# Kernel optimization log

Measured on AMD Instinct MI355X. Metric: run time of the kernel, lower is better.

Reference implementation:

```python
import jax, jax.numpy as jnp
import numpy as np

B, T, C, H = 4, 4096, 1024, 64  # batch, seq_len, n_embd, head_size


def setup_inputs() -> dict:
    key = jax.random.key(0)
    kx, kk, kq, kv = jax.random.split(key, 4)
    x = jax.random.normal(kx, (B, T, C), dtype=jnp.float32)
    Wk = jax.random.normal(kk, (C, H), dtype=jnp.float32) * (C ** -0.5)
    Wq = jax.random.normal(kq, (C, H), dtype=jnp.float32) * (C ** -0.5)
    Wv = jax.random.normal(kv, (C, H), dtype=jnp.float32) * (C ** -0.5)
    return {"x": x, "Wk": Wk, "Wq": Wq, "Wv": Wv}


def reference(x, Wk, Wq, Wv):
    # q,k,v: (B,T,H)
    k = jnp.einsum('btc,ch->bth', x, Wk)
    q = jnp.einsum('btc,ch->bth', x, Wq)
    v = jnp.einsum('btc,ch->bth', x, Wv)
    # NOTE: source scales by C**-0.5 (embedding dim), not head_size**-0.5
    scale = jnp.asarray(C, x.dtype) ** -0.5
    scores = jnp.einsum('bqh,bkh->bqk', q, k) * scale  # (B,T,T)
    causal = jnp.tril(jnp.ones((T, T), dtype=bool))
    scores = jnp.where(causal, scores, jnp.asarray(-jnp.inf, scores.dtype))
    weight = jax.nn.softmax(scores, axis=-1)
    out = jnp.einsum('bqk,bkh->bqh', weight, v)  # (B,T,H)
    return out
```

## Files before the change

### kernel.cpp

```cpp
#include <hip/hip_runtime.h>

typedef unsigned short u16;
typedef unsigned int u32;
typedef float v4f __attribute__((ext_vector_type(4)));
typedef __bf16 v8bf __attribute__((ext_vector_type(8)));

__device__ __forceinline__ u16 f2bf(float f) {
    union { float f; u32 u; } v; v.f = f;
    u32 r = v.u + 0x7fffu + ((v.u >> 16) & 1u);
    return (u16)(r >> 16);
}
__device__ __forceinline__ u32 pk2(float lo, float hi) {
    return ((u32)f2bf(hi) << 16) | (u32)f2bf(lo);
}
__device__ __forceinline__ u32 pk2t(float lo, float hi) {
    union { float f; u32 u; } a, b; a.f = hi; b.f = lo;
    return __builtin_amdgcn_perm(a.u, b.u, 0x07060302u);
}
__device__ __forceinline__ float bfLo(u32 p) {
    union { u32 u; float f; } v; v.u = p << 16; return v.f;
}
__device__ __forceinline__ float bfHi(u32 p) {
    union { u32 u; float f; } v; v.u = p & 0xffff0000u; return v.f;
}
__device__ __forceinline__ v4f zero4() { v4f z = {0.f, 0.f, 0.f, 0.f}; return z; }

__global__ __launch_bounds__(64) void prep_w(const float* __restrict__ Wk,
                                             const float* __restrict__ Wq,
                                             const float* __restrict__ Wv,
                                             u16* __restrict__ WtF) {
    const int f = blockIdx.x >> 5;
    const int ks = blockIdx.x & 31;
    const int lane = threadIdx.x;
    const int w = f >> 2;
    const float* W = (w == 0) ? Wk : ((w == 1) ? Wq : Wv);
    const int h = (f & 3) * 16 + (lane & 15);
    const int k0 = ks * 32 + (lane >> 4) * 8;
    u16 tmp[8];
#pragma unroll
    for (int j = 0; j < 8; ++j) tmp[j] = f2bf(W[(size_t)(k0 + j) * 64 + h]);
    *(uint4*)&WtF[((size_t)blockIdx.x * 64 + lane) * 8] = *(const uint4*)tmp;
}

__global__ __launch_bounds__(256, 2) void qkv_proj(const float* __restrict__ x,
                                                   const u16* __restrict__ WtF,
                                                   u16* __restrict__ qgf,
                                                   u16* __restrict__ Kf,
                                                   u16* __restrict__ Vf) {
    __shared__ v4f red[3][24][64];
    u16* Tk = (u16*)&red[0][0][0];
    u16* Tq = Tk + 32 * 72;
    u16* Tv = Tq + 32 * 72;

    const int tid = threadIdx.x;
    const int lane = tid & 63;
    const int wv = tid >> 6;
    const int l15 = lane & 15, quad = lane >> 4;
    const int row0 = blockIdx.x * 32;

    v4f acc[2][12];
#pragma unroll
    for (int rh = 0; rh < 2; ++rh)
#pragma unroll
        for (int i = 0; i < 12; ++i) acc[rh][i] = zero4();

    union { u32 u[4]; v8bf v; } af[2][8];
#pragma unroll
    for (int rh = 0; rh < 2; ++rh) {
        const float* xr = x + (size_t)(row0 + rh * 16 + l15) * 1024 + wv * 256 + quad * 8;
#pragma unroll
        for (int half = 0; half < 2; ++half) {
            float4 t[8];
#pragma unroll
            for (int i = 0; i < 8; ++i)
                t[i] = *(const float4*)(xr + half * 128 + (i >> 1) * 32 + (i & 1) * 4);
#pragma unroll
            for (int j = 0; j < 4; ++j) {
                int ks = half * 4 + j;
                af[rh][ks].u[0] = pk2(t[2 * j].x, t[2 * j].y);
                af[rh][ks].u[1] = pk2(t[2 * j].z, t[2 * j].w);
                af[rh][ks].u[2] = pk2(t[2 * j + 1].x, t[2 * j + 1].y);
                af[rh][ks].u[3] = pk2(t[2 * j + 1].z, t[2 * j + 1].w);
            }
        }
    }

    const u16* wf0 = WtF + ((size_t)(wv * 8) * 64 + lane) * 8;
#pragma unroll
    for (int f = 0; f < 12; ++f) {
        const u16* wpf = wf0 + (size_t)f * 16384;
#pragma unroll
        for (int ks = 0; ks < 8; ++ks) {
            v8bf bw = *(const v8bf*)(wpf + ks * 512);
            acc[0][f] = __builtin_amdgcn_mfma_f32_16x16x32_bf16(af[0][ks].v, bw,
                                                                acc[0][f], 0, 0, 0);
            acc[1][f] = __builtin_amdgcn_mfma_f32_16x16x32_bf16(af[1][ks].v, bw,
                                                                acc[1][f], 0, 0, 0);
        }
    }

    if (wv > 0) {
#pragma unroll
        for (int rh = 0; rh < 2; ++rh)
#pragma unroll
            for (int f = 0; f < 12; ++f) red[wv - 1][rh * 12 + f][lane] = acc[rh][f];
    }
    __syncthreads();
    if (wv == 0) {
#pragma unroll
        for (int rh = 0; rh < 2; ++rh)
#pragma unroll
            for (int f = 0; f < 12; ++f) {
                acc[rh][f] += red[0][rh * 12 + f][lane];
                acc[rh][f] += red[1][rh * 12 + f][lane];
                acc[rh][f] += red[2][rh * 12 + f][lane];
            }
    }
    __syncthreads();
    if (wv == 0) {
        const float QSC = 0.04508422002778f;
#pragma unroll
        for (int rh = 0; rh < 2; ++rh)
#pragma unroll
            for (int ct = 0; ct < 4; ++ct)
#pragma unroll
                for (int r = 0; r < 4; ++r) {
                    int tok = rh * 16 + quad * 4 + r;
                    Tk[tok * 72 + ct * 16 + l15] = f2bf(acc[rh][ct][r]);
                    Tq[tok * 72 + ct * 16 + l15] = f2bf(acc[rh][ct + 4][r] * QSC);
                    Tv[(ct * 16 + l15) * 40 + tok] = f2bf(acc[rh][ct + 8][r]);
                }
    }
    __syncthreads();

    const int b = row0 >> 12, t0 = row0 & 4095;
    const int kt = t0 >> 6, ct0 = (t0 >> 4) & 3, ksv = (t0 >> 5) & 1;
    const int ln = tid & 63, l15p = ln & 15, qd = ln >> 4;

    {
        int gi = tid >> 7, fi = (tid >> 6) & 1;
        *(uint4*)&qgf[((size_t)((blockIdx.x * 2 + gi) * 2 + fi) * 64 + ln) * 8] =
            *(const uint4*)&Tq[(gi * 16 + l15p) * 72 + fi * 32 + qd * 8];
    }
    {
        int cti = tid >> 7, ks = (tid >> 6) & 1;
        size_t fb = ((((size_t)(b * 64 + kt) * 4 + ct0 + cti) * 2 + ks) * 64 + ln) * 8;
        *(uint4*)&Kf[fb] = *(const uint4*)&Tk[(cti * 16 + l15p) * 72 + ks * 32 + qd * 8];
    }
    {
        int ht = tid >> 6;
        size_t fb = ((((size_t)(b * 64 + kt) * 4 + ht) * 2 + ksv) * 64 + ln) * 8;
        *(uint4*)&Vf[fb] = *(const uint4*)&Tv[(ht * 16 + l15p) * 40 + qd * 8];
    }
}

__global__ __launch_bounds__(128, 3) void attn_part(const u16* __restrict__ qgf,
                                                    const u16* __restrict__ Kf,
                                                    const u16* __restrict__ Vf,
                                                    u32* __restrict__ Opb,
                                                    float* __restrict__ ml,
                                                    int KC, int MAXCH) {
    const int a = blockIdx.x, c = blockIdx.y, b = blockIdx.z;
    if (c * KC > a) return;

    const int tid  = threadIdx.x;
    const int lane = tid & 63;
    const int wv   = tid >> 6;
    const int l15  = lane & 15;
    const int quad = lane >> 4;
    const int q0   = a * 64 + wv * 32;

    const int g0 = (b * 4096 + q0) >> 4;
    v8bf qf[2][2];
#pragma unroll
    for (int st = 0; st < 2; ++st) {
#pragma unroll
        for (int f = 0; f < 2; ++f)
            qf[st][f] = *(const v8bf*)&qgf[((size_t)((g0 + st) * 2 + f) * 64 + lane) * 8];
    }

    union { u32 u[4]; v8bf v; } ones;
    ones.u[0] = ones.u[1] = ones.u[2] = ones.u[3] = 0x3F803F80u;

    v4f o[2][4], l5[2];
#pragma unroll
    for (int st = 0; st < 2; ++st) {
        l5[st] = zero4();
#pragma unroll
        for (int i = 0; i < 4; ++i) o[st][i] = zero4();
    }

    const int kt0 = c * KC;
    const int kt1 = (kt0 + KC < a + 1) ? (kt0 + KC) : (a + 1);

    for (int kt = kt0; kt < kt1; ++kt) {
        const size_t tb = ((size_t)(b * 64 + kt) * 4) * 2 * 512;
        const u16* kp = Kf + tb + lane * 8;
        const u16* vp = Vf + tb + lane * 8;

        v8bf ka[4][2], av[4][2];
#pragma unroll
        for (int ct = 0; ct < 4; ++ct) {
            ka[ct][0] = *(const v8bf*)(kp + (ct * 2 + 0) * 512);
            ka[ct][1] = *(const v8bf*)(kp + (ct * 2 + 1) * 512);
            av[ct][0] = *(const v8bf*)(vp + (ct * 2 + 0) * 512);
            av[ct][1] = *(const v8bf*)(vp + (ct * 2 + 1) * 512);
        }

#pragma unroll
        for (int st = 0; st < 2; ++st) {
            v4f s[4];
#pragma unroll
            for (int ct = 0; ct < 4; ++ct) {
                v4f t = zero4();
                t = __builtin_amdgcn_mfma_f32_16x16x32_bf16(ka[ct][0], qf[st][0], t, 0, 0, 0);
                t = __builtin_amdgcn_mfma_f32_16x16x32_bf16(ka[ct][1], qf[st][1], t, 0, 0, 0);
                s[ct] = t;
            }

            if (kt == a) {
                const int queryg = q0 + st * 16 + l15;
                const int key0 = kt * 64 + quad * 4;
#pragma unroll
                for (int ct = 0; ct < 4; ++ct)
#pragma unroll
                    for (int r = 0; r < 4; ++r)
                        s[ct][r] = ((key0 + ct * 16 + r) > queryg) ? -1e30f : s[ct][r];
            }

            u32 pk[4][2];
#pragma unroll
            for (int ct = 0; ct < 4; ++ct) {
                float p0 = exp2f(s[ct][0]);
                float p1 = exp2f(s[ct][1]);
                float p2 = exp2f(s[ct][2]);
                float p3 = exp2f(s[ct][3]);
                pk[ct][0] = pk2t(p0, p1);
                pk[ct][1] = pk2t(p2, p3);
            }

            const int srcA = ((quad & 1) << 5) + l15;
            const int srcB = srcA + 16;
            const bool hi = (quad >= 2);
#pragma unroll
            for (int ks = 0; ks < 2; ++ks) {
                u32 g0a = (u32)__shfl((int)pk[ks * 2][0], srcA);
                u32 g0b = (u32)__shfl((int)pk[ks * 2 + 1][0], srcA);
                u32 g1a = (u32)__shfl((int)pk[ks * 2][1], srcA);
                u32 g1b = (u32)__shfl((int)pk[ks * 2 + 1][1], srcA);
                u32 g2a = (u32)__shfl((int)pk[ks * 2][0], srcB);
                u32 g2b = (u32)__shfl((int)pk[ks * 2 + 1][0], srcB);
                u32 g3a = (u32)__shfl((int)pk[ks * 2][1], srcB);
                u32 g3b = (u32)__shfl((int)pk[ks * 2 + 1][1], srcB);
                union { u32 u[4]; v8bf v; } pf;
                pf.u[0] = hi ? g0b : g0a;
                pf.u[1] = hi ? g1b : g1a;
                pf.u[2] = hi ? g2b : g2a;
                pf.u[3] = hi ? g3b : g3a;
#pragma unroll
                for (int ht = 0; ht < 4; ++ht)
                    o[st][ht] = __builtin_amdgcn_mfma_f32_16x16x32_bf16(
                        av[ht][ks], pf.v, o[st][ht], 0, 0, 0);
                l5[st] = __builtin_amdgcn_mfma_f32_16x16x32_bf16(
                    ones.v, pf.v, l5[st], 0, 0, 0);
            }
        }
    }

    size_t pidx = ((size_t)b * 64 + a) * MAXCH + c;
    u32* op = Opb + pidx * 2048;
#pragma unroll
    for (int st = 0; st < 2; ++st) {
#pragma unroll
        for (int ht = 0; ht < 2; ++ht)
#pragma unroll
            for (int r = 0; r < 4; ++r)
                op[(ht * 16 + quad * 4 + r) * 64 + wv * 32 + st * 16 + l15] =
                    pk2t(o[st][ht][r], o[st][ht + 2][r]);
        if (quad == 0)
            ml[pidx * 64 + wv * 32 + st * 16 + l15] = l5[st][0];
    }
}

__global__ __launch_bounds__(256) void attn_combine(const u32* __restrict__ Opb,
                                                    const float* __restrict__ ml,
                                                    float* __restrict__ out,
                                                    int KC, int MAXCH) {
    const int a = blockIdx.x, b = blockIdx.y, hz = blockIdx.z;
    const int nch = a / KC + 1;
    const int tid = threadIdx.x;
    const int q = tid & 63, hq = tid >> 6;
    const int h0 = hz * 16 + hq * 4;
    const int rb = h0 & 31;
    const bool hi = (h0 >= 32);
    const size_t pbase = ((size_t)b * 64 + a) * MAXCH;

    float L = 0.f;
    float acc[4] = {0.f, 0.f, 0.f, 0.f};
    for (int c = 0; c < nch; ++c) {
        L += ml[(pbase + c) * 64 + q];
        const u32* op = Opb + (pbase + c) * 2048;
#pragma unroll
        for (int j = 0; j < 4; ++j) {
            u32 v = op[(rb + j) * 64 + q];
            acc[j] += hi ? bfHi(v) : bfLo(v);
        }
    }
    float inv = 1.f / L;
    float4 st = {acc[0] * inv, acc[1] * inv, acc[2] * inv, acc[3] * inv};
    *(float4*)&out[((size_t)b * 4096 + a * 64 + q) * 64 + h0] = st;
}

extern "C" void kernel_launch(void* const* d_in, const int* in_sizes, int n_in,
                              void* d_out, int out_size, void* d_ws, size_t ws_size,
                              hipStream_t stream) {
    const float* x  = (const float*)d_in[0];
    const float* Wk = (const float*)d_in[1];
    const float* Wq = (const float*)d_in[2];
    const float* Wv = (const float*)d_in[3];
    float* out = (float*)d_out;

    char* wsb = (char*)d_ws;
    u16* WtF = (u16*)wsb;
    u16* qgf = (u16*)(wsb + 393216);
    u16* Kf  = (u16*)(wsb + 393216 + 2097152);
    u16* Vf  = (u16*)(wsb + 393216 + 2 * 2097152);
    const size_t base = 393216 + 3 * 2097152;

    int KC = 4, MAXCH = 16;
    while (KC < 64 && base + (size_t)256 * MAXCH * (2048 * 4 + 256) > ws_size) {
        KC <<= 1; MAXCH >>= 1;
    }
    u32* Opb = (u32*)(wsb + base);
    float* ml = (float*)(wsb + base + (size_t)256 * MAXCH * 2048 * 4);

    prep_w<<<dim3(384), dim3(64), 0, stream>>>(Wk, Wq, Wv, WtF);
    qkv_proj<<<dim3(512), dim3(256), 0, stream>>>(x, WtF, qgf, Kf, Vf);
    attn_part<<<dim3(64, MAXCH, 4), dim3(128), 0, stream>>>(qgf, Kf, Vf, Opb, ml, KC, MAXCH);
    attn_combine<<<dim3(64, 4, 4), dim3(256), 0, stream>>>(Opb, ml, out, KC, MAXCH);
}
```

Baseline: 143.2 us.

## Fuse split-K combine into attention kernel via last-block atomic counter

Removes the separate attn_combine launch. Each attention partial block now bumps a per-(batch, query-tile) atomic counter after a threadfence, and the last-arriving chunk block reduces all partials and writes the output. The counters are zeroed in prep_w. This saves a kernel launch and its tail, but the final reduction runs serially in one 128-thread block per tile, with 32 accumulators per thread, and adds fence and atomic overhead.

```diff
diff --git a/kernel.cpp b/kernel.cpp
--- a/kernel.cpp
+++ b/kernel.cpp
@@ -28,10 +28,15 @@
 __global__ __launch_bounds__(64) void prep_w(const float* __restrict__ Wk,
                                              const float* __restrict__ Wq,
                                              const float* __restrict__ Wv,
-                                             u16* __restrict__ WtF) {
+                                             u16* __restrict__ WtF,
+                                             int* __restrict__ cnt) {
+    const int lane = threadIdx.x;
+    if (blockIdx.x == 0) {
+        uint4 z = {0u, 0u, 0u, 0u};
+        ((uint4*)cnt)[lane] = z;
+    }
     const int f = blockIdx.x >> 5;
     const int ks = blockIdx.x & 31;
-    const int lane = threadIdx.x;
     const int w = f >> 2;
     const float* W = (w == 0) ? Wk : ((w == 1) ? Wq : Wv);
     const int h = (f & 3) * 16 + (lane & 15);
@@ -159,7 +164,10 @@
                                                     const u16* __restrict__ Vf,
                                                     u32* __restrict__ Opb,
                                                     float* __restrict__ ml,
+                                                    int* __restrict__ cnt,
+                                                    float* __restrict__ out,
                                                     int KC, int MAXCH) {
+    __shared__ int lastFlag;
     const int a = blockIdx.x, c = blockIdx.y, b = blockIdx.z;
     if (c * KC > a) return;
 
@@ -267,7 +275,8 @@
         }
     }
 
-    size_t pidx = ((size_t)b * 64 + a) * MAXCH + c;
+    const size_t pbase = ((size_t)b * 64 + a) * MAXCH;
+    const size_t pidx = pbase + c;
     u32* op = Opb + pidx * 2048;
 #pragma unroll
     for (int st = 0; st < 2; ++st) {
@@ -280,35 +289,44 @@
         if (quad == 0)
             ml[pidx * 64 + wv * 32 + st * 16 + l15] = l5[st][0];
     }
-}
-
-__global__ __launch_bounds__(256) void attn_combine(const u32* __restrict__ Opb,
-                                                    const float* __restrict__ ml,
-                                                    float* __restrict__ out,
-                                                    int KC, int MAXCH) {
-    const int a = blockIdx.x, b = blockIdx.y, hz = blockIdx.z;
+
     const int nch = a / KC + 1;
-    const int tid = threadIdx.x;
-    const int q = tid & 63, hq = tid >> 6;
-    const int h0 = hz * 16 + hq * 4;
-    const int rb = h0 & 31;
-    const bool hi = (h0 >= 32);
-    const size_t pbase = ((size_t)b * 64 + a) * MAXCH;
-
+    __threadfence();
+    __syncthreads();
+    if (tid == 0) {
+        int old = atomicAdd(&cnt[b * 64 + a], 1);
+        lastFlag = (old == nch - 1) ? 1 : 0;
+    }
+    __syncthreads();
+    if (!lastFlag) return;
+    __threadfence();
+
+    const int q = tid & 63, hg = tid >> 6;
     float L = 0.f;
-    float acc[4] = {0.f, 0.f, 0.f, 0.f};
-    for (int c = 0; c < nch; ++c) {
-        L += ml[(pbase + c) * 64 + q];
-        const u32* op = Opb + (pbase + c) * 2048;
-#pragma unroll
-        for (int j = 0; j < 4; ++j) {
-            u32 v = op[(rb + j) * 64 + q];
-            acc[j] += hi ? bfHi(v) : bfLo(v);
-        }
-    }
-    float inv = 1.f / L;
-    float4 st = {acc[0] * inv, acc[1] * inv, acc[2] * inv, acc[3] * inv};
-    *(float4*)&out[((size_t)b * 4096 + a * 64 + q) * 64 + h0] = st;
+    float accL[16], accH[16];
+#pragma unroll
+    for (int j = 0; j < 16; ++j) { accL[j] = 0.f; accH[j] = 0.f; }
+    for (int ch = 0; ch < nch; ++ch) {
+        L += ml[(pbase + ch) * 64 + q];
+        const u32* op2 = Opb + (pbase + ch) * 2048;
+#pragma unroll
+        for (int j = 0; j < 16; ++j) {
+            u32 v = op2[(hg * 16 + j) * 64 + q];
+            accL[j] += bfLo(v);
+            accH[j] += bfHi(v);
+        }
+    }
+    const float inv = 1.f / L;
+    float* orow = out + ((size_t)b * 4096 + a * 64 + q) * 64 + hg * 16;
+#pragma unroll
+    for (int j4 = 0; j4 < 4; ++j4) {
+        float4 lo4 = {accL[4 * j4] * inv, accL[4 * j4 + 1] * inv,
+                      accL[4 * j4 + 2] * inv, accL[4 * j4 + 3] * inv};
+        float4 hi4 = {accH[4 * j4] * inv, accH[4 * j4 + 1] * inv,
+                      accH[4 * j4 + 2] * inv, accH[4 * j4 + 3] * inv};
+        *(float4*)(orow + 4 * j4) = lo4;
+        *(float4*)(orow + 32 + 4 * j4) = hi4;
+    }
 }
 
 extern "C" void kernel_launch(void* const* d_in, const int* in_sizes, int n_in,
@@ -328,14 +346,14 @@
     const size_t base = 393216 + 3 * 2097152;
 
     int KC = 4, MAXCH = 16;
-    while (KC < 64 && base + (size_t)256 * MAXCH * (2048 * 4 + 256) > ws_size) {
+    while (KC < 64 && base + (size_t)256 * MAXCH * (2048 * 4 + 256) + 1024 > ws_size) {
         KC <<= 1; MAXCH >>= 1;
     }
     u32* Opb = (u32*)(wsb + base);
     float* ml = (float*)(wsb + base + (size_t)256 * MAXCH * 2048 * 4);
-
-    prep_w<<<dim3(384), dim3(64), 0, stream>>>(Wk, Wq, Wv, WtF);
+    int* cnt = (int*)(wsb + base + (size_t)256 * MAXCH * (2048 * 4 + 256));
+
+    prep_w<<<dim3(384), dim3(64), 0, stream>>>(Wk, Wq, Wv, WtF, cnt);
     qkv_proj<<<dim3(512), dim3(256), 0, stream>>>(x, WtF, qgf, Kf, Vf);
-    attn_part<<<dim3(64, MAXCH, 4), dim3(128), 0, stream>>>(qgf, Kf, Vf, Opb, ml, KC, MAXCH);
-    attn_combine<<<dim3(64, 4, 4), dim3(256), 0, stream>>>(Opb, ml, out, KC, MAXCH);
-}
+    attn_part<<<dim3(64, MAXCH, 4), dim3(128), 0, stream>>>(qgf, Kf, Vf, Opb, ml, cnt, out, KC, MAXCH);
+}
```

Result: slower. 313.5 us (+118.9%).
